# Kernel tuning notes

Measured on AMD Instinct MI355X. Metric: run time of the kernel, lower is better.

The kernel has to match this reference:

```python
import jax, jax.numpy as jnp
import numpy as np

B, S, D, F, E = 4, 2048, 512, 2048, 8  # batch, seq, d_model, d_ff, n_experts


def setup_inputs() -> dict:
    key = jax.random.key(0)
    k = jax.random.split(key, 5)
    x = jax.random.normal(k[0], (B, S, D), dtype=jnp.float32)
    Ws = jax.random.normal(k[1], (D, E), dtype=jnp.float32) * 0.02  # router weight
    bs = jnp.zeros((E,), dtype=jnp.float32)
    W1 = jax.random.normal(k[2], (E, D, F), dtype=jnp.float32) * 0.02
    b1 = jnp.zeros((E, F), dtype=jnp.float32)
    W2 = jax.random.normal(k[3], (E, F, D), dtype=jnp.float32) * 0.02
    b2 = jnp.zeros((E, D), dtype=jnp.float32)
    return {"x": x, "Ws": Ws, "bs": bs, "W1": W1, "b1": b1, "W2": W2, "b2": b2}


def reference(x, Ws, bs, W1, b1, W2, b2):
    # x: [B, S, D]. The torch module permutes in and permutes back, so the
    # batch/seq layout is preserved end to end; flatten to tokens [T, D].
    Bb, Ss, Dd = x.shape
    xt = x.reshape(-1, Dd)                       # [T, D]
    logits = xt @ Ws + bs                        # [T, E]
    probs = jax.nn.softmax(logits, axis=-1)
    prob_max = jnp.max(probs, axis=-1)           # [T] top-1 routing prob
    routes = jnp.argmax(probs, axis=-1)          # [T] expert ids
    onehot = jax.nn.one_hot(routes, W1.shape[0], dtype=xt.dtype)  # [T, E]

    # Per-expert FFN (eval mode: dropout is identity). drop_tokens=False, so
    # every token is processed by its routed expert. Dense dispatch: each
    # expert runs on all tokens, combine selects the routed output per token.
    def expert_ffn(w1, bb1, w2, bb2):
        h = jax.nn.gelu(xt @ w1 + bb1, approximate=False)  # [T, F] exact GELU (nn.GELU default)
        return h @ w2 + bb2                                # [T, D]

    y = jax.vmap(expert_ffn)(W1, b1, W2, b2)     # [E, T, D]
    out = jnp.einsum("te,etd->td", onehot, y)    # combine (scatter of routed outputs)
    out = out * prob_max[:, None]                # is_scale_prob=True
    return out.reshape(Bb, Ss, Dd)
```

## Files before the change

### kernel.cpp

```cpp
#include <hip/hip_runtime.h>
#include <hip/hip_fp16.h>
#include <cmath>

#define Tn 8192
#define Dn 512
#define Fn 2048
#define En 8

typedef _Float16 f16x8 __attribute__((ext_vector_type(8)));
typedef _Float16 f16x4 __attribute__((ext_vector_type(4)));
typedef float f32x4 __attribute__((ext_vector_type(4)));

#define MAXTILES 136

__device__ __forceinline__ void gload16(const void* g, void* l) {
    __builtin_amdgcn_global_load_lds(
        (const __attribute__((address_space(1))) unsigned int*)g,
        (__attribute__((address_space(3))) unsigned int*)l, 16, 0, 0);
}

__device__ __forceinline__ float fast_gelu(float v) {
    float z = fabsf(v) * 0.70710678118654752f;
    float t = 1.0f / fmaf(0.3275911f, z, 1.0f);
    float p = t * fmaf(t, fmaf(t, fmaf(t, fmaf(t, 1.061405429f, -1.453152027f),
                                       1.421413741f), -0.284496736f), 0.254829592f);
    float e = __expf(-z * z);
    float erfa = fmaf(-p, e, 1.0f);
    float phi = 0.5f + copysignf(0.5f * erfa, v);
    return v * phi;
}

__global__ __launch_bounds__(256) void prep_kernel(
    const float* __restrict__ x, const float* __restrict__ Ws,
    const float* __restrict__ bs, _Float16* __restrict__ x16,
    int* __restrict__ route, float* __restrict__ scale,
    int* __restrict__ poslocal, int* __restrict__ blockCounts,
    const float* __restrict__ W1, const float* __restrict__ W2,
    _Float16* __restrict__ W1T, _Float16* __restrict__ W2T)
{
    __shared__ float tilebuf[64][65];
    __shared__ int hist[8];
    const int tid = threadIdx.x;

    if (blockIdx.x < 256) {
        if (tid < 8) hist[tid] = 0;
        __syncthreads();

        const int lane = tid & 63;
        const int w = tid >> 6;
        const int tokBase = blockIdx.x * 32 + w * 8;

        float wreg[8][8];
#pragma unroll
        for (int j = 0; j < 4; ++j) {
            const float4* p = reinterpret_cast<const float4*>(Ws + (4 * lane + j) * En);
            float4 a = p[0], b = p[1];
            wreg[j][0] = a.x; wreg[j][1] = a.y; wreg[j][2] = a.z; wreg[j][3] = a.w;
            wreg[j][4] = b.x; wreg[j][5] = b.y; wreg[j][6] = b.z; wreg[j][7] = b.w;
        }
#pragma unroll
        for (int j = 0; j < 4; ++j) {
            const float4* p = reinterpret_cast<const float4*>(Ws + (256 + 4 * lane + j) * En);
            float4 a = p[0], b = p[1];
            wreg[4 + j][0] = a.x; wreg[4 + j][1] = a.y; wreg[4 + j][2] = a.z; wreg[4 + j][3] = a.w;
            wreg[4 + j][4] = b.x; wreg[4 + j][5] = b.y; wreg[4 + j][6] = b.z; wreg[4 + j][7] = b.w;
        }
        float bsv[8];
#pragma unroll
        for (int e = 0; e < 8; ++e) bsv[e] = bs[e];

        for (int it = 0; it < 8; ++it) {
            int t = tokBase + it;
            const float4* xr = reinterpret_cast<const float4*>(x + (size_t)t * Dn);
            float4 v0 = xr[lane];
            float4 v1 = xr[64 + lane];
            f16x4 h0, h1;
            h0[0] = (_Float16)v0.x; h0[1] = (_Float16)v0.y; h0[2] = (_Float16)v0.z; h0[3] = (_Float16)v0.w;
            h1[0] = (_Float16)v1.x; h1[1] = (_Float16)v1.y; h1[2] = (_Float16)v1.z; h1[3] = (_Float16)v1.w;
            *reinterpret_cast<f16x4*>(x16 + (size_t)t * Dn + 4 * lane) = h0;
            *reinterpret_cast<f16x4*>(x16 + (size_t)t * Dn + 256 + 4 * lane) = h1;

            float xv[8] = {v0.x, v0.y, v0.z, v0.w, v1.x, v1.y, v1.z, v1.w};
            float part[8];
#pragma unroll
            for (int e = 0; e < 8; ++e) part[e] = 0.f;
#pragma unroll
            for (int j = 0; j < 8; ++j)
#pragma unroll
                for (int e = 0; e < 8; ++e) part[e] = fmaf(xv[j], wreg[j][e], part[e]);
#pragma unroll
            for (int s = 32; s > 0; s >>= 1) {
#pragma unroll
                for (int e = 0; e < 8; ++e) part[e] += __shfl_xor(part[e], s);
            }
            if (lane == 0) {
                float lg[8];
                lg[0] = part[0] + bsv[0];
                float m = lg[0]; int am = 0;
#pragma unroll
                for (int e = 1; e < 8; ++e) {
                    lg[e] = part[e] + bsv[e];
                    if (lg[e] > m) { m = lg[e]; am = e; }
                }
                float sum = 0.f;
#pragma unroll
                for (int e = 0; e < 8; ++e) sum += expf(lg[e] - m);
                route[t] = am;
                scale[t] = 1.0f / sum;
                poslocal[t] = atomicAdd(&hist[am], 1);
            }
        }
        __syncthreads();
        if (tid < 8) blockCounts[blockIdx.x * 8 + tid] = hist[tid];
        return;
    }

    int bx = blockIdx.x - 256;
    const float* in; _Float16* outp; int R, C, tR, tC;
    if (bx < 2048) {
        int e = bx >> 8, t = bx & 255;
        R = Dn; C = Fn; tR = t >> 5; tC = t & 31;
        in = W1 + (size_t)e * Dn * Fn;
        outp = W1T + (size_t)e * Dn * Fn;
    } else {
        int b2 = bx - 2048;
        int e = b2 >> 8, t = b2 & 255;
        R = Fn; C = Dn; tR = t >> 3; tC = t & 7;
        in = W2 + (size_t)e * Fn * Dn;
        outp = W2T + (size_t)e * Fn * Dn;
    }
    int r0 = tR * 64, c0 = tC * 64;
    int row = tid >> 2, cq = tid & 3;
#pragma unroll
    for (int i = 0; i < 4; ++i) {
        float4 v = *reinterpret_cast<const float4*>(in + (size_t)(r0 + row) * C + c0 + cq * 16 + i * 4);
        tilebuf[row][cq * 16 + i * 4 + 0] = v.x;
        tilebuf[row][cq * 16 + i * 4 + 1] = v.y;
        tilebuf[row][cq * 16 + i * 4 + 2] = v.z;
        tilebuf[row][cq * 16 + i * 4 + 3] = v.w;
    }
    __syncthreads();
    int col = tid >> 2, rq = tid & 3;
    f16x8 o0, o1;
#pragma unroll
    for (int i = 0; i < 8; ++i) o0[i] = (_Float16)tilebuf[rq * 16 + i][col];
#pragma unroll
    for (int i = 0; i < 8; ++i) o1[i] = (_Float16)tilebuf[rq * 16 + 8 + i][col];
    size_t base = (size_t)(c0 + col) * R + r0 + rq * 16;
    *reinterpret_cast<f16x8*>(outp + base) = o0;
    *reinterpret_cast<f16x8*>(outp + base + 8) = o1;
}

__global__ __launch_bounds__(256) void plan_kernel(
    const int* __restrict__ blockCounts,
    int* __restrict__ base,
    int* __restrict__ nTiles, int* __restrict__ tileExpert,
    int* __restrict__ tileBase, int* __restrict__ tileEnd)
{
    __shared__ int cnt[256 * 8];
    __shared__ int groupSum[32 * 8];
    __shared__ int groupBase[32 * 8];
    __shared__ int totals[8];
    __shared__ int offsets_s[8];
    const int tid = threadIdx.x;
    for (int i = tid; i < 2048; i += 256) cnt[i] = blockCounts[i];
    __syncthreads();
    const int e = tid & 7, g = tid >> 3;
    {
        int s = 0;
#pragma unroll
        for (int b = g * 8; b < g * 8 + 8; ++b) s += cnt[b * 8 + e];
        groupSum[g * 8 + e] = s;
    }
    __syncthreads();
    if (tid < 8) {
        int run = 0;
        for (int gg = 0; gg < 32; ++gg) {
            groupBase[gg * 8 + tid] = run;
            run += groupSum[gg * 8 + tid];
        }
        totals[tid] = run;
    }
    __syncthreads();
    if (tid == 0) {
        int off = 0, nt = 0;
        for (int ee = 0; ee < En; ++ee) {
            offsets_s[ee] = off;
            int c = totals[ee];
            int tiles = (c + 63) / 64;
            for (int r = 0; r < tiles; ++r) {
                tileExpert[nt] = ee;
                tileBase[nt] = off + r * 64;
                tileEnd[nt] = off + c;
                ++nt;
            }
            off += c;
        }
        *nTiles = nt;
    }
    __syncthreads();
    {
        int run = offsets_s[e] + groupBase[g * 8 + e];
#pragma unroll
        for (int b = g * 8; b < g * 8 + 8; ++b) {
            base[b * 8 + e] = run;
            run += cnt[b * 8 + e];
        }
    }
}

__global__ __launch_bounds__(256) void scatter_kernel(
    const int* __restrict__ route, const int* __restrict__ poslocal,
    const int* __restrict__ base, int* __restrict__ order)
{
    int t = blockIdx.x * 256 + threadIdx.x;
    if (t >= Tn) return;
    int e = route[t];
    int rb = t >> 5;
    order[base[rb * 8 + e] + poslocal[t]] = t;
}

__global__ __launch_bounds__(64) void gemm1_kernel(
    const _Float16* __restrict__ x16, const _Float16* __restrict__ W1T,
    const float* __restrict__ b1, const int* __restrict__ order,
    const int* __restrict__ nTiles, const int* __restrict__ tileExpert,
    const int* __restrict__ tileBase, const int* __restrict__ tileEnd,
    _Float16* __restrict__ hbuf)
{
    __shared__ _Float16 As[64 * 64];
    __shared__ _Float16 Bs[64 * 64];
    const int bx = blockIdx.x;
    const int bt = (bx & 7) * 17 + (bx >> 3);
    if (bt >= *nTiles) return;
    const int e = tileExpert[bt], rowBase = tileBase[bt], rowEnd = tileEnd[bt];
    const int nBase = blockIdx.y * 64;
    const int lane = threadIdx.x;

    const int swc = ((lane & 7) ^ (lane >> 3)) * 8;
    const _Float16* Asrc[8];
    const _Float16* Bsrc[8];
#pragma unroll
    for (int p = 0; p < 8; ++p) {
        int r = p * 8 + (lane >> 3);
        int tok = order[min(rowBase + r, Tn - 1)];
        Asrc[p] = x16 + (size_t)tok * Dn + swc;
        Bsrc[p] = W1T + (size_t)e * Dn * Fn + (size_t)(nBase + r) * Dn + swc;
    }

#define STAGE1(kt) do {                                                  \
        _Pragma("unroll")                                                \
        for (int p = 0; p < 8; ++p) {                                    \
            gload16(Asrc[p] + (kt) * 64, As + (p * 64 + lane) * 8);      \
            gload16(Bsrc[p] + (kt) * 64, Bs + (p * 64 + lane) * 8);      \
        }                                                                \
    } while (0)

    const int fr = lane & 15;
    const int off0 = (((lane >> 4))     ^ (lane & 7)) * 8;
    const int off1 = ((4 + (lane >> 4)) ^ (lane & 7)) * 8;

    f32x4 acc[4][4];
#pragma unroll
    for (int m = 0; m < 4; ++m)
#pragma unroll
        for (int n = 0; n < 4; ++n) acc[m][n] = {0.f, 0.f, 0.f, 0.f};

    STAGE1(0);
    const int NKT = Dn / 64;
    for (int kt = 0; kt < NKT; ++kt) {
        asm volatile("s_waitcnt vmcnt(0)" ::: "memory");
        f16x8 af[4][2], bf[4][2];
#pragma unroll
        for (int m = 0; m < 4; ++m) {
            af[m][0] = *reinterpret_cast<const f16x8*>(As + (m * 16 + fr) * 64 + off0);
            af[m][1] = *reinterpret_cast<const f16x8*>(As + (m * 16 + fr) * 64 + off1);
        }
#pragma unroll
        for (int n = 0; n < 4; ++n) {
            bf[n][0] = *reinterpret_cast<const f16x8*>(Bs + (n * 16 + fr) * 64 + off0);
            bf[n][1] = *reinterpret_cast<const f16x8*>(Bs + (n * 16 + fr) * 64 + off1);
        }
        asm volatile("s_waitcnt lgkmcnt(0)" ::: "memory");
        if (kt + 1 < NKT) STAGE1(kt + 1);
        __builtin_amdgcn_s_setprio(1);
#pragma unroll
        for (int ks = 0; ks < 2; ++ks)
#pragma unroll
            for (int m = 0; m < 4; ++m)
#pragma unroll
                for (int n = 0; n < 4; ++n)
                    acc[m][n] = __builtin_amdgcn_mfma_f32_16x16x32_f16(af[m][ks], bf[n][ks], acc[m][n], 0, 0, 0);
        __builtin_amdgcn_s_setprio(0);
    }
#undef STAGE1

    float b1v[4];
#pragma unroll
    for (int n = 0; n < 4; ++n) b1v[n] = b1[(size_t)e * Fn + nBase + n * 16 + fr];
#pragma unroll
    for (int m = 0; m < 4; ++m) {
#pragma unroll
        for (int j = 0; j < 4; ++j) {
            int i = rowBase + m * 16 + (lane >> 4) * 4 + j;
            if (i < rowEnd) {
#pragma unroll
                for (int n = 0; n < 4; ++n) {
                    float g = fast_gelu(acc[m][n][j] + b1v[n]);
                    hbuf[(size_t)i * Fn + nBase + n * 16 + fr] = (_Float16)g;
                }
            }
        }
    }
}

__global__ __launch_bounds__(64) void gemm2_kernel(
    const _Float16* __restrict__ hbuf, const _Float16* __restrict__ W2T,
    const float* __restrict__ b2, const int* __restrict__ order,
    const float* __restrict__ scale,
    const int* __restrict__ nTiles, const int* __restrict__ tileExpert,
    const int* __restrict__ tileBase, const int* __restrict__ tileEnd,
    float* __restrict__ out)
{
    __shared__ _Float16 As[64 * 64];
    __shared__ _Float16 Bs[64 * 64];
    const int bx = blockIdx.x;
    const int bt = (bx & 7) * 17 + (bx >> 3);
    if (bt >= *nTiles) return;
    const int e = tileExpert[bt], rowBase = tileBase[bt], rowEnd = tileEnd[bt];
    const int nBase = blockIdx.y * 64;
    const int lane = threadIdx.x;

    const int swc = ((lane & 7) ^ (lane >> 3)) * 8;
    const _Float16* Asrc[8];
    const _Float16* Bsrc[8];
#pragma unroll
    for (int p = 0; p < 8; ++p) {
        int r = p * 8 + (lane >> 3);
        Asrc[p] = hbuf + (size_t)min(rowBase + r, Tn - 1) * Fn + swc;
        Bsrc[p] = W2T + (size_t)e * Fn * Dn + (size_t)(nBase + r) * Fn + swc;
    }

#define STAGE2(kt) do {                                                  \
        _Pragma("unroll")                                                \
        for (int p = 0; p < 8; ++p) {                                    \
            gload16(Asrc[p] + (kt) * 64, As + (p * 64 + lane) * 8);      \
            gload16(Bsrc[p] + (kt) * 64, Bs + (p * 64 + lane) * 8);      \
        }                                                                \
    } while (0)

    const int fr = lane & 15;
    const int off0 = (((lane >> 4))     ^ (lane & 7)) * 8;
    const int off1 = ((4 + (lane >> 4)) ^ (lane & 7)) * 8;

    f32x4 acc[4][4];
#pragma unroll
    for (int m = 0; m < 4; ++m)
#pragma unroll
        for (int n = 0; n < 4; ++n) acc[m][n] = {0.f, 0.f, 0.f, 0.f};

    STAGE2(0);
    const int NKT = Fn / 64;
    for (int kt = 0; kt < NKT; ++kt) {
        asm volatile("s_waitcnt vmcnt(0)" ::: "memory");
        f16x8 af[4][2], bf[4][2];
#pragma unroll
        for (int m = 0; m < 4; ++m) {
            af[m][0] = *reinterpret_cast<const f16x8*>(As + (m * 16 + fr) * 64 + off0);
            af[m][1] = *reinterpret_cast<const f16x8*>(As + (m * 16 + fr) * 64 + off1);
        }
#pragma unroll
        for (int n = 0; n < 4; ++n) {
            bf[n][0] = *reinterpret_cast<const f16x8*>(Bs + (n * 16 + fr) * 64 + off0);
            bf[n][1] = *reinterpret_cast<const f16x8*>(Bs + (n * 16 + fr) * 64 + off1);
        }
        asm volatile("s_waitcnt lgkmcnt(0)" ::: "memory");
        if (kt + 1 < NKT) STAGE2(kt + 1);
        __builtin_amdgcn_s_setprio(1);
#pragma unroll
        for (int ks = 0; ks < 2; ++ks)
#pragma unroll
            for (int m = 0; m < 4; ++m)
#pragma unroll
                for (int n = 0; n < 4; ++n)
                    acc[m][n] = __builtin_amdgcn_mfma_f32_16x16x32_f16(af[m][ks], bf[n][ks], acc[m][n], 0, 0, 0);
        __builtin_amdgcn_s_setprio(0);
    }
#undef STAGE2

    float b2v[4];
#pragma unroll
    for (int n = 0; n < 4; ++n) b2v[n] = b2[(size_t)e * Dn + nBase + n * 16 + fr];
#pragma unroll
    for (int m = 0; m < 4; ++m) {
#pragma unroll
        for (int j = 0; j < 4; ++j) {
            int i = rowBase + m * 16 + (lane >> 4) * 4 + j;
            if (i < rowEnd) {
                int tok = order[i];
                float s = scale[tok];
#pragma unroll
                for (int n = 0; n < 4; ++n)
                    out[(size_t)tok * Dn + nBase + n * 16 + fr] = (acc[m][n][j] + b2v[n]) * s;
            }
        }
    }
}

extern "C" void kernel_launch(void* const* d_in, const int* in_sizes, int n_in,
                              void* d_out, int out_size, void* d_ws, size_t ws_size,
                              hipStream_t stream) {
    const float* x  = (const float*)d_in[0];
    const float* Ws = (const float*)d_in[1];
    const float* bs = (const float*)d_in[2];
    const float* W1 = (const float*)d_in[3];
    const float* b1 = (const float*)d_in[4];
    const float* W2 = (const float*)d_in[5];
    const float* b2 = (const float*)d_in[6];
    float* out = (float*)d_out;

    char* ws = (char*)d_ws;
    int* nTiles      = (int*)(ws + 0);
    int* tileExpert  = (int*)(ws + 256);
    int* tileBase    = (int*)(ws + 1024);
    int* tileEnd     = (int*)(ws + 2048);
    int* route       = (int*)(ws + 4096);
    float* scale     = (float*)(ws + 4096 + 4 * Tn);
    int* poslocal    = (int*)(ws + 4096 + 8 * Tn);
    int* order       = (int*)(ws + 4096 + 12 * Tn);
    int* blockCounts = (int*)(ws + 4096 + 16 * Tn);
    int* base        = (int*)(ws + 4096 + 16 * Tn + 8192);
    _Float16* x16    = (_Float16*)(ws + (1 << 20));
    _Float16* W1T    = x16 + (size_t)Tn * Dn;
    _Float16* W2T    = W1T + (size_t)En * Dn * Fn;
    _Float16* hbuf   = W2T + (size_t)En * Fn * Dn;

    prep_kernel<<<256 + 4096, 256, 0, stream>>>(x, Ws, bs, x16, route, scale, poslocal,
                                                blockCounts, W1, W2, W1T, W2T);
    plan_kernel<<<1, 256, 0, stream>>>(blockCounts, base, nTiles, tileExpert, tileBase, tileEnd);
    scatter_kernel<<<Tn / 256, 256, 0, stream>>>(route, poslocal, base, order);
    gemm1_kernel<<<dim3(MAXTILES, Fn / 64), 64, 0, stream>>>(
        x16, W1T, b1, order, nTiles, tileExpert, tileBase, tileEnd, hbuf);
    gemm2_kernel<<<dim3(MAXTILES, Dn / 64), 64, 0, stream>>>(
        hbuf, W2T, b2, order, scale, nTiles, tileExpert, tileBase, tileEnd, out);
}
```

Baseline: 112.2 us.

## Double-buffer LDS with K=32 stages in both expert GEMMs

Both grouped GEMM kernels now use two 64x32 LDS buffers per operand instead of one 64x64 buffer. Loads run two K-steps ahead, with a partial vmcnt wait so the next tile's global loads overlap the current MFMAs. The smaller K chunk doubles the number of loop iterations and waits, and it needs a new XOR swizzle for the narrower rows.

```diff
diff --git a/kernel.cpp b/kernel.cpp
--- a/kernel.cpp
+++ b/kernel.cpp
@@ -227,8 +227,8 @@
     const int* __restrict__ tileBase, const int* __restrict__ tileEnd,
     _Float16* __restrict__ hbuf)
 {
-    __shared__ _Float16 As[64 * 64];
-    __shared__ _Float16 Bs[64 * 64];
+    __shared__ _Float16 As[2 * 64 * 32];
+    __shared__ _Float16 Bs[2 * 64 * 32];
     const int bx = blockIdx.x;
     const int bt = (bx & 7) * 17 + (bx >> 3);
     if (bt >= *nTiles) return;
@@ -236,28 +236,27 @@
     const int nBase = blockIdx.y * 64;
     const int lane = threadIdx.x;
 
-    const int swc = ((lane & 7) ^ (lane >> 3)) * 8;
-    const _Float16* Asrc[8];
-    const _Float16* Bsrc[8];
-#pragma unroll
-    for (int p = 0; p < 8; ++p) {
-        int r = p * 8 + (lane >> 3);
+    const int swc = ((lane & 3) ^ ((lane >> 3) & 3)) * 8;
+    const _Float16* Asrc[4];
+    const _Float16* Bsrc[4];
+#pragma unroll
+    for (int p = 0; p < 4; ++p) {
+        int r = p * 16 + (lane >> 2);
         int tok = order[min(rowBase + r, Tn - 1)];
         Asrc[p] = x16 + (size_t)tok * Dn + swc;
         Bsrc[p] = W1T + (size_t)e * Dn * Fn + (size_t)(nBase + r) * Dn + swc;
     }
 
-#define STAGE1(kt) do {                                                  \
-        _Pragma("unroll")                                                \
-        for (int p = 0; p < 8; ++p) {                                    \
-            gload16(Asrc[p] + (kt) * 64, As + (p * 64 + lane) * 8);      \
-            gload16(Bsrc[p] + (kt) * 64, Bs + (p * 64 + lane) * 8);      \
-        }                                                                \
+#define STAGE1(b, kt) do {                                                \
+        _Pragma("unroll")                                                 \
+        for (int p = 0; p < 4; ++p) {                                     \
+            gload16(Asrc[p] + (kt) * 32, As + (b) * 2048 + p * 512 + lane * 8); \
+            gload16(Bsrc[p] + (kt) * 32, Bs + (b) * 2048 + p * 512 + lane * 8); \
+        }                                                                 \
     } while (0)
 
     const int fr = lane & 15;
-    const int off0 = (((lane >> 4))     ^ (lane & 7)) * 8;
-    const int off1 = ((4 + (lane >> 4)) ^ (lane & 7)) * 8;
+    const int co = (((lane >> 4)) ^ ((fr >> 1) & 3)) * 8;
 
     f32x4 acc[4][4];
 #pragma unroll
@@ -265,31 +264,28 @@
 #pragma unroll
         for (int n = 0; n < 4; ++n) acc[m][n] = {0.f, 0.f, 0.f, 0.f};
 
-    STAGE1(0);
-    const int NKT = Dn / 64;
+    STAGE1(0, 0);
+    STAGE1(1, 1);
+    const int NKT = Dn / 32;
     for (int kt = 0; kt < NKT; ++kt) {
-        asm volatile("s_waitcnt vmcnt(0)" ::: "memory");
-        f16x8 af[4][2], bf[4][2];
-#pragma unroll
-        for (int m = 0; m < 4; ++m) {
-            af[m][0] = *reinterpret_cast<const f16x8*>(As + (m * 16 + fr) * 64 + off0);
-            af[m][1] = *reinterpret_cast<const f16x8*>(As + (m * 16 + fr) * 64 + off1);
-        }
-#pragma unroll
-        for (int n = 0; n < 4; ++n) {
-            bf[n][0] = *reinterpret_cast<const f16x8*>(Bs + (n * 16 + fr) * 64 + off0);
-            bf[n][1] = *reinterpret_cast<const f16x8*>(Bs + (n * 16 + fr) * 64 + off1);
-        }
+        const int cur = kt & 1;
+        if (kt + 1 < NKT) asm volatile("s_waitcnt vmcnt(8)" ::: "memory");
+        else              asm volatile("s_waitcnt vmcnt(0)" ::: "memory");
+        f16x8 af[4], bf[4];
+#pragma unroll
+        for (int m = 0; m < 4; ++m)
+            af[m] = *reinterpret_cast<const f16x8*>(As + cur * 2048 + (m * 16 + fr) * 32 + co);
+#pragma unroll
+        for (int n = 0; n < 4; ++n)
+            bf[n] = *reinterpret_cast<const f16x8*>(Bs + cur * 2048 + (n * 16 + fr) * 32 + co);
         asm volatile("s_waitcnt lgkmcnt(0)" ::: "memory");
-        if (kt + 1 < NKT) STAGE1(kt + 1);
+        if (kt + 2 < NKT) STAGE1(cur, kt + 2);
         __builtin_amdgcn_s_setprio(1);
 #pragma unroll
-        for (int ks = 0; ks < 2; ++ks)
-#pragma unroll
-            for (int m = 0; m < 4; ++m)
-#pragma unroll
-                for (int n = 0; n < 4; ++n)
-                    acc[m][n] = __builtin_amdgcn_mfma_f32_16x16x32_f16(af[m][ks], bf[n][ks], acc[m][n], 0, 0, 0);
+        for (int m = 0; m < 4; ++m)
+#pragma unroll
+            for (int n = 0; n < 4; ++n)
+                acc[m][n] = __builtin_amdgcn_mfma_f32_16x16x32_f16(af[m], bf[n], acc[m][n], 0, 0, 0);
         __builtin_amdgcn_s_setprio(0);
     }
 #undef STAGE1
@@ -321,8 +317,8 @@
     const int* __restrict__ tileBase, const int* __restrict__ tileEnd,
     float* __restrict__ out)
 {
-    __shared__ _Float16 As[64 * 64];
-    __shared__ _Float16 Bs[64 * 64];
+    __shared__ _Float16 As[2 * 64 * 32];
+    __shared__ _Float16 Bs[2 * 64 * 32];
     const int bx = blockIdx.x;
     const int bt = (bx & 7) * 17 + (bx >> 3);
     if (bt >= *nTiles) return;
@@ -330,27 +326,26 @@
     const int nBase = blockIdx.y * 64;
     const int lane = threadIdx.x;
 
-    const int swc = ((lane & 7) ^ (lane >> 3)) * 8;
-    const _Float16* Asrc[8];
-    const _Float16* Bsrc[8];
-#pragma unroll
-    for (int p = 0; p < 8; ++p) {
-        int r = p * 8 + (lane >> 3);
+    const int swc = ((lane & 3) ^ ((lane >> 3) & 3)) * 8;
+    const _Float16* Asrc[4];
+    const _Float16* Bsrc[4];
+#pragma unroll
+    for (int p = 0; p < 4; ++p) {
+        int r = p * 16 + (lane >> 2);
         Asrc[p] = hbuf + (size_t)min(rowBase + r, Tn - 1) * Fn + swc;
         Bsrc[p] = W2T + (size_t)e * Fn * Dn + (size_t)(nBase + r) * Fn + swc;
     }
 
-#define STAGE2(kt) do {                                                  \
-        _Pragma("unroll")                                                \
-        for (int p = 0; p < 8; ++p) {                                    \
-            gload16(Asrc[p] + (kt) * 64, As + (p * 64 + lane) * 8);      \
-            gload16(Bsrc[p] + (kt) * 64, Bs + (p * 64 + lane) * 8);      \
-        }                                                                \
+#define STAGE2(b, kt) do {                                                \
+        _Pragma("unroll")                                                 \
+        for (int p = 0; p < 4; ++p) {                                     \
+            gload16(Asrc[p] + (kt) * 32, As + (b) * 2048 + p * 512 + lane * 8); \
+            gload16(Bsrc[p] + (kt) * 32, Bs + (b) * 2048 + p * 512 + lane * 8); \
+        }                                                                 \
     } while (0)
 
     const int fr = lane & 15;
-    const int off0 = (((lane >> 4))     ^ (lane & 7)) * 8;
-    const int off1 = ((4 + (lane >> 4)) ^ (lane & 7)) * 8;
+    const int co = (((lane >> 4)) ^ ((fr >> 1) & 3)) * 8;
 
     f32x4 acc[4][4];
 #pragma unroll
@@ -358,31 +353,28 @@
 #pragma unroll
         for (int n = 0; n < 4; ++n) acc[m][n] = {0.f, 0.f, 0.f, 0.f};
 
-    STAGE2(0);
-    const int NKT = Fn / 64;
+    STAGE2(0, 0);
+    STAGE2(1, 1);
+    const int NKT = Fn / 32;
     for (int kt = 0; kt < NKT; ++kt) {
-        asm volatile("s_waitcnt vmcnt(0)" ::: "memory");
-        f16x8 af[4][2], bf[4][2];
-#pragma unroll
-        for (int m = 0; m < 4; ++m) {
-            af[m][0] = *reinterpret_cast<const f16x8*>(As + (m * 16 + fr) * 64 + off0);
-            af[m][1] = *reinterpret_cast<const f16x8*>(As + (m * 16 + fr) * 64 + off1);
-        }
-#pragma unroll
-        for (int n = 0; n < 4; ++n) {
-            bf[n][0] = *reinterpret_cast<const f16x8*>(Bs + (n * 16 + fr) * 64 + off0);
-            bf[n][1] = *reinterpret_cast<const f16x8*>(Bs + (n * 16 + fr) * 64 + off1);
-        }
+        const int cur = kt & 1;
+        if (kt + 1 < NKT) asm volatile("s_waitcnt vmcnt(8)" ::: "memory");
+        else              asm volatile("s_waitcnt vmcnt(0)" ::: "memory");
+        f16x8 af[4], bf[4];
+#pragma unroll
+        for (int m = 0; m < 4; ++m)
+            af[m] = *reinterpret_cast<const f16x8*>(As + cur * 2048 + (m * 16 + fr) * 32 + co);
+#pragma unroll
+        for (int n = 0; n < 4; ++n)
+            bf[n] = *reinterpret_cast<const f16x8*>(Bs + cur * 2048 + (n * 16 + fr) * 32 + co);
         asm volatile("s_waitcnt lgkmcnt(0)" ::: "memory");
-        if (kt + 1 < NKT) STAGE2(kt + 1);
+        if (kt + 2 < NKT) STAGE2(cur, kt + 2);
         __builtin_amdgcn_s_setprio(1);
 #pragma unroll
-        for (int ks = 0; ks < 2; ++ks)
-#pragma unroll
-            for (int m = 0; m < 4; ++m)
-#pragma unroll
-                for (int n = 0; n < 4; ++n)
-                    acc[m][n] = __builtin_amdgcn_mfma_f32_16x16x32_f16(af[m][ks], bf[n][ks], acc[m][n], 0, 0, 0);
+        for (int m = 0; m < 4; ++m)
+#pragma unroll
+            for (int n = 0; n < 4; ++n)
+                acc[m][n] = __builtin_amdgcn_mfma_f32_16x16x32_f16(af[m], bf[n], acc[m][n], 0, 0, 0);
         __builtin_amdgcn_s_setprio(0);
     }
 #undef STAGE2
```

New measurement: 137.1 us. 1.22x slower.

## Double-buffer LDS tiles in expert GEMMs with partial vmcnt waits

Applied to the files above, without the earlier changes.

Both expert GEMM kernels now use two LDS buffers per operand, each holding one 64-wide K half of a 128-wide K step. Loads for the next step are issued into one buffer while the MFMA phases consume the other, and waits use vmcnt(16) instead of draining all loads. The goal is to hide global-to-LDS latency behind compute in these single-wave blocks. The cost is twice the LDS per block, which may reduce occupancy, and more complex wait-count bookkeeping.

```diff
diff --git a/kernel.cpp b/kernel.cpp
--- a/kernel.cpp
+++ b/kernel.cpp
@@ -227,8 +227,10 @@
     const int* __restrict__ tileBase, const int* __restrict__ tileEnd,
     _Float16* __restrict__ hbuf)
 {
-    __shared__ _Float16 As[64 * 64];
-    __shared__ _Float16 Bs[64 * 64];
+    __shared__ _Float16 As0[64 * 64];
+    __shared__ _Float16 As1[64 * 64];
+    __shared__ _Float16 Bs0[64 * 64];
+    __shared__ _Float16 Bs1[64 * 64];
     const int bx = blockIdx.x;
     const int bt = (bx & 7) * 17 + (bx >> 3);
     if (bt >= *nTiles) return;
@@ -247,17 +249,45 @@
         Bsrc[p] = W1T + (size_t)e * Dn * Fn + (size_t)(nBase + r) * Dn + swc;
     }
 
-#define STAGE1(kt) do {                                                  \
-        _Pragma("unroll")                                                \
-        for (int p = 0; p < 8; ++p) {                                    \
-            gload16(Asrc[p] + (kt) * 64, As + (p * 64 + lane) * 8);      \
-            gload16(Bsrc[p] + (kt) * 64, Bs + (p * 64 + lane) * 8);      \
-        }                                                                \
+#define SH0(kt) do {                                                      \
+        _Pragma("unroll")                                                 \
+        for (int p = 0; p < 8; ++p) {                                     \
+            gload16(Asrc[p] + (kt) * 128, As0 + p * 512 + lane * 8);      \
+            gload16(Bsrc[p] + (kt) * 128, Bs0 + p * 512 + lane * 8);      \
+        }                                                                 \
     } while (0)
+#define SH1(kt) do {                                                      \
+        _Pragma("unroll")                                                 \
+        for (int p = 0; p < 8; ++p) {                                     \
+            gload16(Asrc[p] + (kt) * 128 + 64, As1 + p * 512 + lane * 8); \
+            gload16(Bsrc[p] + (kt) * 128 + 64, Bs1 + p * 512 + lane * 8); \
+        }                                                                 \
+    } while (0)
 
     const int fr = lane & 15;
-    const int off0 = (((lane >> 4))     ^ (lane & 7)) * 8;
-    const int off1 = ((4 + (lane >> 4)) ^ (lane & 7)) * 8;
+    const int kg = lane >> 4;
+    const int f7 = fr & 7;
+    const int co0 = (kg ^ f7) * 8;
+    const int co1 = ((4 + kg) ^ f7) * 8;
+
+#define PH1(AH, BH, CO, STG) do {                                               \
+        f16x8 af[4], bf[4];                                                     \
+        _Pragma("unroll")                                                       \
+        for (int m = 0; m < 4; ++m)                                             \
+            af[m] = *reinterpret_cast<const f16x8*>((AH) + (m * 16 + fr) * 64 + (CO)); \
+        _Pragma("unroll")                                                       \
+        for (int n = 0; n < 4; ++n)                                             \
+            bf[n] = *reinterpret_cast<const f16x8*>((BH) + (n * 16 + fr) * 64 + (CO)); \
+        asm volatile("s_waitcnt lgkmcnt(0)" ::: "memory");                      \
+        STG;                                                                    \
+        __builtin_amdgcn_s_setprio(1);                                          \
+        _Pragma("unroll")                                                       \
+        for (int m = 0; m < 4; ++m)                                             \
+            _Pragma("unroll")                                                   \
+            for (int n = 0; n < 4; ++n)                                         \
+                acc[m][n] = __builtin_amdgcn_mfma_f32_16x16x32_f16(af[m], bf[n], acc[m][n], 0, 0, 0); \
+        __builtin_amdgcn_s_setprio(0);                                          \
+    } while (0)
 
     f32x4 acc[4][4];
 #pragma unroll
@@ -265,34 +295,21 @@
 #pragma unroll
         for (int n = 0; n < 4; ++n) acc[m][n] = {0.f, 0.f, 0.f, 0.f};
 
-    STAGE1(0);
-    const int NKT = Dn / 64;
+    SH0(0);
+    SH1(0);
+    const int NKT = Dn / 128;
     for (int kt = 0; kt < NKT; ++kt) {
-        asm volatile("s_waitcnt vmcnt(0)" ::: "memory");
-        f16x8 af[4][2], bf[4][2];
-#pragma unroll
-        for (int m = 0; m < 4; ++m) {
-            af[m][0] = *reinterpret_cast<const f16x8*>(As + (m * 16 + fr) * 64 + off0);
-            af[m][1] = *reinterpret_cast<const f16x8*>(As + (m * 16 + fr) * 64 + off1);
-        }
-#pragma unroll
-        for (int n = 0; n < 4; ++n) {
-            bf[n][0] = *reinterpret_cast<const f16x8*>(Bs + (n * 16 + fr) * 64 + off0);
-            bf[n][1] = *reinterpret_cast<const f16x8*>(Bs + (n * 16 + fr) * 64 + off1);
-        }
-        asm volatile("s_waitcnt lgkmcnt(0)" ::: "memory");
-        if (kt + 1 < NKT) STAGE1(kt + 1);
-        __builtin_amdgcn_s_setprio(1);
-#pragma unroll
-        for (int ks = 0; ks < 2; ++ks)
-#pragma unroll
-            for (int m = 0; m < 4; ++m)
-#pragma unroll
-                for (int n = 0; n < 4; ++n)
-                    acc[m][n] = __builtin_amdgcn_mfma_f32_16x16x32_f16(af[m][ks], bf[n][ks], acc[m][n], 0, 0, 0);
-        __builtin_amdgcn_s_setprio(0);
-    }
-#undef STAGE1
+        const bool more = (kt + 1 < NKT);
+        asm volatile("s_waitcnt vmcnt(16)" ::: "memory");
+        PH1(As0, Bs0, co0, );
+        PH1(As0, Bs0, co1, if (more) SH0(kt + 1));
+        if (more) asm volatile("s_waitcnt vmcnt(16)" ::: "memory");
+        else      asm volatile("s_waitcnt vmcnt(0)" ::: "memory");
+        PH1(As1, Bs1, co0, );
+        PH1(As1, Bs1, co1, if (more) SH1(kt + 1));
+    }
+#undef SH0
+#undef SH1
 
     float b1v[4];
 #pragma unroll
@@ -321,8 +338,10 @@
     const int* __restrict__ tileBase, const int* __restrict__ tileEnd,
     float* __restrict__ out)
 {
-    __shared__ _Float16 As[64 * 64];
-    __shared__ _Float16 Bs[64 * 64];
+    __shared__ _Float16 As0[64 * 64];
+    __shared__ _Float16 As1[64 * 64];
+    __shared__ _Float16 Bs0[64 * 64];
+    __shared__ _Float16 Bs1[64 * 64];
     const int bx = blockIdx.x;
     const int bt = (bx & 7) * 17 + (bx >> 3);
     if (bt >= *nTiles) return;
@@ -340,17 +359,26 @@
         Bsrc[p] = W2T + (size_t)e * Fn * Dn + (size_t)(nBase + r) * Fn + swc;
     }
 
-#define STAGE2(kt) do {                                                  \
-        _Pragma("unroll")                                                \
-        for (int p = 0; p < 8; ++p) {                                    \
-            gload16(Asrc[p] + (kt) * 64, As + (p * 64 + lane) * 8);      \
-            gload16(Bsrc[p] + (kt) * 64, Bs + (p * 64 + lane) * 8);      \
-        }                                                                \
+#define SH0(kt) do {                                                      \
+        _Pragma("unroll")                                                 \
+        for (int p = 0; p < 8; ++p) {                                     \
+            gload16(Asrc[p] + (kt) * 128, As0 + p * 512 + lane * 8);      \
+            gload16(Bsrc[p] + (kt) * 128, Bs0 + p * 512 + lane * 8);      \
+        }                                                                 \
     } while (0)
+#define SH1(kt) do {                                                      \
+        _Pragma("unroll")                                                 \
+        for (int p = 0; p < 8; ++p) {                                     \
+            gload16(Asrc[p] + (kt) * 128 + 64, As1 + p * 512 + lane * 8); \
+            gload16(Bsrc[p] + (kt) * 128 + 64, Bs1 + p * 512 + lane * 8); \
+        }                                                                 \
+    } while (0)
 
     const int fr = lane & 15;
-    const int off0 = (((lane >> 4))     ^ (lane & 7)) * 8;
-    const int off1 = ((4 + (lane >> 4)) ^ (lane & 7)) * 8;
+    const int kg = lane >> 4;
+    const int f7 = fr & 7;
+    const int co0 = (kg ^ f7) * 8;
+    const int co1 = ((4 + kg) ^ f7) * 8;
 
     f32x4 acc[4][4];
 #pragma unroll
@@ -358,34 +386,21 @@
 #pragma unroll
         for (int n = 0; n < 4; ++n) acc[m][n] = {0.f, 0.f, 0.f, 0.f};
 
-    STAGE2(0);
-    const int NKT = Fn / 64;
+    SH0(0);
+    SH1(0);
+    const int NKT = Fn / 128;
     for (int kt = 0; kt < NKT; ++kt) {
-        asm volatile("s_waitcnt vmcnt(0)" ::: "memory");
-        f16x8 af[4][2], bf[4][2];
-#pragma unroll
-        for (int m = 0; m < 4; ++m) {
-            af[m][0] = *reinterpret_cast<const f16x8*>(As + (m * 16 + fr) * 64 + off0);
-            af[m][1] = *reinterpret_cast<const f16x8*>(As + (m * 16 + fr) * 64 + off1);
-        }
-#pragma unroll
-        for (int n = 0; n < 4; ++n) {
-            bf[n][0] = *reinterpret_cast<const f16x8*>(Bs + (n * 16 + fr) * 64 + off0);
-            bf[n][1] = *reinterpret_cast<const f16x8*>(Bs + (n * 16 + fr) * 64 + off1);
-        }
-        asm volatile("s_waitcnt lgkmcnt(0)" ::: "memory");
-        if (kt + 1 < NKT) STAGE2(kt + 1);
-        __builtin_amdgcn_s_setprio(1);
-#pragma unroll
-        for (int ks = 0; ks < 2; ++ks)
-#pragma unroll
-            for (int m = 0; m < 4; ++m)
-#pragma unroll
-                for (int n = 0; n < 4; ++n)
-                    acc[m][n] = __builtin_amdgcn_mfma_f32_16x16x32_f16(af[m][ks], bf[n][ks], acc[m][n], 0, 0, 0);
-        __builtin_amdgcn_s_setprio(0);
-    }
-#undef STAGE2
+        const bool more = (kt + 1 < NKT);
+        asm volatile("s_waitcnt vmcnt(16)" ::: "memory");
+        PH1(As0, Bs0, co0, );
+        PH1(As0, Bs0, co1, if (more) SH0(kt + 1));
+        if (more) asm volatile("s_waitcnt vmcnt(16)" ::: "memory");
+        else      asm volatile("s_waitcnt vmcnt(0)" ::: "memory");
+        PH1(As1, Bs1, co0, );
+        PH1(As1, Bs1, co1, if (more) SH1(kt + 1));
+    }
+#undef SH0
+#undef SH1
 
     float b2v[4];
 #pragma unroll
```

New measurement: 150.5 us. 1.34x slower.
